# Performance work log

Measured on AMD Instinct MI355X. Metric: run time of the kernel, lower is better.

Reference implementation:

```python
import jax, jax.numpy as jnp
import numpy as np

WBITS = 4
ABITS = 8
OBITS = 8


def fwht(x):
    """Normalized fast Walsh-Hadamard transform along the last axis (n power of 2).
    Equivalent to matmul_hadU with had_K = I, K = 1 (n = 4096 = 2^12)."""
    shape = x.shape
    n = shape[-1]
    x = x.reshape(-1, n)
    h = 1
    while h < n:
        x = x.reshape(-1, n // (2 * h), 2, h)
        a, b = x[:, :, 0, :], x[:, :, 1, :]
        x = jnp.concatenate([a + b, a - b], axis=-1).reshape(-1, n)
        h *= 2
    inv_sqrt_n = jnp.asarray(1.0 / np.sqrt(n), x.dtype)
    return (x * inv_sqrt_n).reshape(shape)


def sym_fake_quant(t, bits, axis):
    """Symmetric min-max RTN fake quantization (per-channel for weights,
    per-token for activations)."""
    qmax = jnp.asarray(2.0 ** (bits - 1) - 1.0, t.dtype)
    scale = jnp.max(jnp.abs(t), axis=axis, keepdims=True) / qmax
    scale = jnp.maximum(scale, jnp.asarray(1e-8, t.dtype))
    q = jnp.clip(jnp.round(t / scale), -qmax, qmax)
    return q * scale


def setup_inputs() -> dict:
    key = jax.random.key(0)
    k1, k2, k3 = jax.random.split(key, 3)
    B, S, DIN, DOUT = 4, 2048, 4096, 4096
    return {
        "input": jax.random.normal(k1, (B, S, DIN), dtype=jnp.float32),
        "weight": jax.random.normal(k2, (DOUT, DIN), dtype=jnp.float32) * 0.02,
        "bias": jax.random.normal(k3, (DOUT,), dtype=jnp.float32) * 0.01,
    }


def reference(input, weight, bias):
    # online full Hadamard rotation of activations
    x = fwht(input)
    # activation quant (per-token, symmetric int8 fake-quant)
    x = sym_fake_quant(x, ABITS, axis=-1)
    # weight quant (per-output-channel, symmetric int4 fake-quant)
    w = sym_fake_quant(weight, WBITS, axis=-1)
    # F.linear: x @ w.T + b
    out = jnp.einsum("bsi,oi->bso", x, w) + bias
    # output quant (per-token, symmetric int8 fake-quant)
    out = sym_fake_quant(out, OBITS, axis=-1)
    return out
```

## Files before the change

kernel.cpp:

```cpp
#include <hip/hip_runtime.h>
#include <hip/hip_bf16.h>

#define DIN 4096
#define DOUT 4096
#define NROWS 8192

typedef int i32x4 __attribute__((ext_vector_type(4)));

__device__ __forceinline__ float block_absmax(float m, float* red) {
  #pragma unroll
  for (int off = 32; off > 0; off >>= 1)
    m = fmaxf(m, __shfl_down(m, off));
  const int tid = threadIdx.x;
  if ((tid & 63) == 0) red[tid >> 6] = m;
  __syncthreads();
  return fmaxf(fmaxf(red[0], red[1]), fmaxf(red[2], red[3]));
}

__global__ __launch_bounds__(256) void fwht_quant_kernel(
    const float* __restrict__ in, char* __restrict__ qx,
    float* __restrict__ sx) {
  __shared__ float buf[DIN];
  __shared__ float red[4];
  const int tid = threadIdx.x;
  const size_t row = blockIdx.x;
  const float4* src = (const float4*)(in + row * DIN);
  float4* b4 = (float4*)buf;
  for (int i = tid; i < DIN / 4; i += 256) b4[i] = src[i];
  __syncthreads();
  for (int h = 1; h < DIN; h <<= 1) {
    #pragma unroll
    for (int s = 0; s < 8; ++s) {
      int t = tid + s * 256;
      int i0 = ((t & ~(h - 1)) << 1) | (t & (h - 1));
      int i1 = i0 + h;
      float a = buf[i0], b = buf[i1];
      buf[i0] = a + b;
      buf[i1] = a - b;
    }
    __syncthreads();
  }
  const float inv = 0.015625f;
  float m = 0.0f;
  for (int i = tid; i < DIN / 4; i += 256) {
    float4 v = b4[i];
    m = fmaxf(m, fmaxf(fmaxf(fabsf(v.x), fabsf(v.y)),
                       fmaxf(fabsf(v.z), fabsf(v.w))));
  }
  float mx = block_absmax(m, red) * inv;
  float scale = fmaxf(mx / 127.0f, 1e-8f);
  if (tid == 0) sx[row] = scale;
  char* dst = qx + row * DIN;
  const float rs = 1.0f / scale;
  for (int i0 = tid * 4; i0 < DIN; i0 += 1024) {
    char4 pk;
    float q0 = fminf(fmaxf(rintf((buf[i0 + 0] * inv) * rs), -127.f), 127.f);
    float q1 = fminf(fmaxf(rintf((buf[i0 + 1] * inv) * rs), -127.f), 127.f);
    float q2 = fminf(fmaxf(rintf((buf[i0 + 2] * inv) * rs), -127.f), 127.f);
    float q3 = fminf(fmaxf(rintf((buf[i0 + 3] * inv) * rs), -127.f), 127.f);
    pk.x = (char)q0; pk.y = (char)q1; pk.z = (char)q2; pk.w = (char)q3;
    *(char4*)(dst + i0) = pk;
  }
}

__global__ __launch_bounds__(256) void wquant_kernel(
    const float* __restrict__ w, char* __restrict__ qw,
    float* __restrict__ sw) {
  __shared__ float buf[DIN];
  __shared__ float red[4];
  const int tid = threadIdx.x;
  const size_t row = blockIdx.x;
  const float4* src = (const float4*)(w + row * DIN);
  float4* b4 = (float4*)buf;
  float m = 0.0f;
  for (int i = tid; i < DIN / 4; i += 256) {
    float4 v = src[i];
    b4[i] = v;
    m = fmaxf(m, fmaxf(fmaxf(fabsf(v.x), fabsf(v.y)),
                       fmaxf(fabsf(v.z), fabsf(v.w))));
  }
  float mx = block_absmax(m, red);
  float scale = fmaxf(mx / 7.0f, 1e-8f);
  if (tid == 0) sw[row] = scale;
  char* dst = qw + row * DIN;
  const float rs = 1.0f / scale;
  for (int i0 = tid * 4; i0 < DIN; i0 += 1024) {
    char4 pk;
    float q0 = fminf(fmaxf(rintf(buf[i0 + 0] * rs), -7.f), 7.f);
    float q1 = fminf(fmaxf(rintf(buf[i0 + 1] * rs), -7.f), 7.f);
    float q2 = fminf(fmaxf(rintf(buf[i0 + 2] * rs), -7.f), 7.f);
    float q3 = fminf(fmaxf(rintf(buf[i0 + 3] * rs), -7.f), 7.f);
    pk.x = (char)q0; pk.y = (char)q1; pk.z = (char)q2; pk.w = (char)q3;
    *(char4*)(dst + i0) = pk;
  }
}

__global__ __launch_bounds__(512, 2) void gemm_kernel(
    const char* __restrict__ A,
    const char* __restrict__ Bt,
    const float* __restrict__ sx, const float* __restrict__ sw,
    const float* __restrict__ bias, float* __restrict__ out) {
  __shared__ char lds[131072];
  const int tid = threadIdx.x;
  const int lane = tid & 63;
  const int wid = tid >> 6;
  const int wr = wid >> 2;
  const int wc = wid & 3;
  int bid = blockIdx.x;
  int swz = (bid & 7) * 64 + (bid >> 3);
  const int tm = swz >> 4;
  const int tn = swz & 15;
  const size_t row0 = (size_t)tm * 256;
  const size_t col0 = (size_t)tn * 256;
  const int slot0 = (((lane >> 4) ^ (lane & 7)) << 4);

  i32x4 acc[4][2][4] = {};
  i32x4 fb[4][2];
  i32x4 fa[2][2];

#define STAGE(MAT, GROW0, KT, LBASE)                                          \
  {                                                                           \
    _Pragma("unroll")                                                         \
    for (int j = 0; j < 2; ++j) {                                             \
      int chunk = j * 8 + wid;                                                \
      int rr = chunk * 8 + (lane >> 3);                                       \
      int cc = (KT) * 128 + (((lane & 7) ^ (lane >> 3)) << 4);                \
      const char* src = (MAT) + ((GROW0) + rr) * (size_t)DIN + cc;            \
      __builtin_amdgcn_global_load_lds(                                       \
          (const __attribute__((address_space(1))) void*)src,                 \
          (__attribute__((address_space(3))) void*)(lds + (LBASE) +           \
                                                    chunk * 1024),            \
          16, 0, 0);                                                          \
    }                                                                         \
  }
#define STAGE_A(P, HALF, KT) \
  STAGE(A, row0 + (HALF) * 128, KT, (P) * 32768 + (HALF) * 16384)
#define STAGE_B(P, HALF, KT) \
  STAGE(Bt, col0 + (HALF) * 128, KT, 65536 + (P) * 32768 + (HALF) * 16384)

#define DS_A(Q, P)                                                            \
  {                                                                           \
    _Pragma("unroll")                                                         \
    for (int mm = 0; mm < 2; ++mm) {                                          \
      int ar = (Q) * 64 + wr * 32 + mm * 16 + (lane & 15);                    \
      _Pragma("unroll")                                                       \
      for (int kk = 0; kk < 2; ++kk)                                          \
        fa[mm][kk] =                                                          \
            *(const i32x4*)(lds + (P) * 32768 + ar * 128 + (slot0 ^ (kk * 64))); \
    }                                                                         \
  }
#define DS_B(P)                                                               \
  {                                                                           \
    _Pragma("unroll")                                                         \
    for (int nn = 0; nn < 4; ++nn) {                                          \
      int br = wc * 64 + nn * 16 + (lane & 15);                               \
      _Pragma("unroll")                                                       \
      for (int kk = 0; kk < 2; ++kk)                                          \
        fb[nn][kk] = *(const i32x4*)(lds + 65536 + (P) * 32768 + br * 128 +   \
                                     (slot0 ^ (kk * 64)));                    \
    }                                                                         \
  }
#define MFMA16(Q)                                                             \
  {                                                                           \
    __builtin_amdgcn_s_setprio(1);                                            \
    _Pragma("unroll")                                                         \
    for (int kk = 0; kk < 2; ++kk)                                            \
      _Pragma("unroll")                                                       \
      for (int mm = 0; mm < 2; ++mm)                                          \
        _Pragma("unroll")                                                     \
        for (int nn = 0; nn < 4; ++nn)                                        \
          acc[Q][mm][nn] = __builtin_amdgcn_mfma_i32_16x16x64_i8(             \
              fa[mm][kk], fb[nn][kk], acc[Q][mm][nn], 0, 0, 0);               \
    __builtin_amdgcn_s_setprio(0);                                            \
  }
#define BAR() __builtin_amdgcn_s_barrier()
#define WAIT_LGKM0() asm volatile("s_waitcnt lgkmcnt(0)" ::: "memory")

  STAGE_B(0, 0, 0); STAGE_B(0, 1, 0); STAGE_A(0, 0, 0); STAGE_A(0, 1, 0);
  STAGE_B(1, 0, 1); STAGE_B(1, 1, 1); STAGE_A(1, 0, 1);
  asm volatile("s_waitcnt vmcnt(6)" ::: "memory");
  BAR();

  #pragma unroll 1
  for (int i = 0; i < 16; ++i) {
    const int a = 2 * i, b = 2 * i + 1;
    const bool nl = (i < 15);
    DS_A(0, 0); DS_B(0);
    STAGE_A(1, 1, b);
    asm volatile("s_waitcnt lgkmcnt(8)" ::: "memory");
    BAR(); WAIT_LGKM0();
    MFMA16(0);
    BAR();
    DS_A(1, 0);
    if (nl) STAGE_B(0, 0, a + 2);
    BAR(); WAIT_LGKM0();
    MFMA16(1);
    BAR();
    DS_A(2, 0);
    if (nl) STAGE_B(0, 1, a + 2);
    BAR(); WAIT_LGKM0();
    MFMA16(2);
    BAR();
    DS_A(3, 0);
    if (nl) STAGE_A(0, 0, a + 2);
    BAR(); WAIT_LGKM0();
    MFMA16(3);
    if (nl) { asm volatile("s_waitcnt vmcnt(6)" ::: "memory"); }
    else    { asm volatile("s_waitcnt vmcnt(0)" ::: "memory"); }
    BAR();
    DS_A(0, 1); DS_B(1);
    if (nl) STAGE_A(0, 1, a + 2);
    asm volatile("s_waitcnt lgkmcnt(8)" ::: "memory");
    BAR(); WAIT_LGKM0();
    MFMA16(0);
    BAR();
    DS_A(1, 1);
    if (nl) STAGE_B(1, 0, b + 2);
    BAR(); WAIT_LGKM0();
    MFMA16(1);
    BAR();
    DS_A(2, 1);
    if (nl) STAGE_B(1, 1, b + 2);
    BAR(); WAIT_LGKM0();
    MFMA16(2);
    BAR();
    DS_A(3, 1);
    if (nl) STAGE_A(1, 0, b + 2);
    BAR(); WAIT_LGKM0();
    MFMA16(3);
    if (nl) { asm volatile("s_waitcnt vmcnt(6)" ::: "memory"); }
    BAR();
  }

  float swv[4], bv[4];
  #pragma unroll
  for (int nn = 0; nn < 4; ++nn) {
    size_t gc = col0 + wc * 64 + nn * 16 + (lane & 15);
    swv[nn] = sw[gc];
    bv[nn] = bias[gc];
  }
  #pragma unroll
  for (int q = 0; q < 4; ++q) {
    #pragma unroll
    for (int mm = 0; mm < 2; ++mm) {
      #pragma unroll
      for (int j = 0; j < 4; ++j) {
        size_t gr = row0 + q * 64 + wr * 32 + mm * 16 + ((lane >> 4) << 2) + j;
        float sxr = sx[gr];
        float* orow = out + gr * DOUT + col0 + wc * 64 + (lane & 15);
        #pragma unroll
        for (int nn = 0; nn < 4; ++nn)
          orow[nn * 16] = (float)acc[q][mm][nn][j] * (sxr * swv[nn]) + bv[nn];
      }
    }
  }
#undef STAGE
#undef STAGE_A
#undef STAGE_B
#undef DS_A
#undef DS_B
#undef MFMA16
#undef BAR
#undef WAIT_LGKM0
}

__global__ __launch_bounds__(256) void rowquant_kernel(float* __restrict__ out) {
  __shared__ float buf[DOUT];
  __shared__ float red[4];
  const int tid = threadIdx.x;
  const size_t row = blockIdx.x;
  float4* g4 = (float4*)(out + row * DOUT);
  float4* b4 = (float4*)buf;
  float m = 0.0f;
  for (int i = tid; i < DOUT / 4; i += 256) {
    float4 v = g4[i];
    b4[i] = v;
    m = fmaxf(m, fmaxf(fmaxf(fabsf(v.x), fabsf(v.y)),
                       fmaxf(fabsf(v.z), fabsf(v.w))));
  }
  float mx = block_absmax(m, red);
  float scale = fmaxf(mx / 127.0f, 1e-8f);
  for (int i = tid; i < DOUT / 4; i += 256) {
    float4 v = b4[i];
    v.x = fminf(fmaxf(rintf(v.x / scale), -127.0f), 127.0f) * scale;
    v.y = fminf(fmaxf(rintf(v.y / scale), -127.0f), 127.0f) * scale;
    v.z = fminf(fmaxf(rintf(v.z / scale), -127.0f), 127.0f) * scale;
    v.w = fminf(fmaxf(rintf(v.w / scale), -127.0f), 127.0f) * scale;
    g4[i] = v;
  }
}

extern "C" void kernel_launch(void* const* d_in, const int* in_sizes, int n_in,
                              void* d_out, int out_size, void* d_ws, size_t ws_size,
                              hipStream_t stream) {
  (void)in_sizes; (void)n_in; (void)out_size; (void)ws_size;
  const float* input = (const float*)d_in[0];
  const float* weight = (const float*)d_in[1];
  const float* bias = (const float*)d_in[2];
  float* out = (float*)d_out;
  char* ws = (char*)d_ws;
  char* qx = ws;
  char* qw = ws + ((size_t)32 << 20);
  float* sx = (float*)(ws + ((size_t)48 << 20));
  float* sw = (float*)(ws + ((size_t)48 << 20) + ((size_t)32 << 10));

  fwht_quant_kernel<<<NROWS, 256, 0, stream>>>(input, qx, sx);
  wquant_kernel<<<DOUT, 256, 0, stream>>>(weight, qw, sw);
  gemm_kernel<<<512, 512, 0, stream>>>(qx, qw, sx, sw, bias, out);
  rowquant_kernel<<<NROWS, 256, 0, stream>>>(out);
}
```

Before: 264.6 us.

## Register-resident radix-16 FWHT, coarser GEMM phases, register rowquant

```diff
diff --git a/kernel.cpp b/kernel.cpp
--- a/kernel.cpp
+++ b/kernel.cpp
@@ -20,47 +20,71 @@
 __global__ __launch_bounds__(256) void fwht_quant_kernel(
     const float* __restrict__ in, char* __restrict__ qx,
     float* __restrict__ sx) {
-  __shared__ float buf[DIN];
+  __shared__ float lds[4352];
   __shared__ float red[4];
   const int tid = threadIdx.x;
   const size_t row = blockIdx.x;
+  const int th = tid >> 4, tl = tid & 15;
+  float v[16];
+
   const float4* src = (const float4*)(in + row * DIN);
-  float4* b4 = (float4*)buf;
-  for (int i = tid; i < DIN / 4; i += 256) b4[i] = src[i];
+  #pragma unroll
+  for (int k = 0; k < 4; ++k) {
+    float4 f = src[tid * 4 + k];
+    v[4 * k + 0] = f.x; v[4 * k + 1] = f.y;
+    v[4 * k + 2] = f.z; v[4 * k + 3] = f.w;
+  }
+  #pragma unroll
+  for (int hb = 1; hb < 16; hb <<= 1)
+    #pragma unroll
+    for (int j = 0; j < 16; ++j)
+      if (!(j & hb)) {
+        float a0 = v[j], b0 = v[j | hb];
+        v[j] = a0 + b0; v[j | hb] = a0 - b0;
+      }
+  #pragma unroll
+  for (int j = 0; j < 16; ++j) lds[17 * tid + j] = v[j];
   __syncthreads();
-  for (int h = 1; h < DIN; h <<= 1) {
+  #pragma unroll
+  for (int j = 0; j < 16; ++j) v[j] = lds[272 * th + 17 * j + tl];
+  #pragma unroll
+  for (int hb = 1; hb < 16; hb <<= 1)
     #pragma unroll
-    for (int s = 0; s < 8; ++s) {
-      int t = tid + s * 256;
-      int i0 = ((t & ~(h - 1)) << 1) | (t & (h - 1));
-      int i1 = i0 + h;
-      float a = buf[i0], b = buf[i1];
-      buf[i0] = a + b;
-      buf[i1] = a - b;
-    }
-    __syncthreads();
-  }
-  const float inv = 0.015625f;
+    for (int j = 0; j < 16; ++j)
+      if (!(j & hb)) {
+        float a0 = v[j], b0 = v[j | hb];
+        v[j] = a0 + b0; v[j | hb] = a0 - b0;
+      }
+  #pragma unroll
+  for (int j = 0; j < 16; ++j) lds[272 * th + 17 * j + tl] = v[j];
+  __syncthreads();
+  #pragma unroll
+  for (int j = 0; j < 16; ++j) v[j] = lds[272 * j + 17 * th + tl];
+  #pragma unroll
+  for (int hb = 1; hb < 16; hb <<= 1)
+    #pragma unroll
+    for (int j = 0; j < 16; ++j)
+      if (!(j & hb)) {
+        float a0 = v[j], b0 = v[j | hb];
+        v[j] = a0 + b0; v[j | hb] = a0 - b0;
+      }
   float m = 0.0f;
-  for (int i = tid; i < DIN / 4; i += 256) {
-    float4 v = b4[i];
-    m = fmaxf(m, fmaxf(fmaxf(fabsf(v.x), fabsf(v.y)),
-                       fmaxf(fabsf(v.z), fabsf(v.w))));
-  }
-  float mx = block_absmax(m, red) * inv;
+  #pragma unroll
+  for (int j = 0; j < 16; ++j) m = fmaxf(m, fabsf(v[j]));
+  #pragma unroll
+  for (int j = 0; j < 16; ++j) lds[272 * j + 17 * th + tl] = v[j];
+  float mx = block_absmax(m, red) * 0.015625f;
   float scale = fmaxf(mx / 127.0f, 1e-8f);
   if (tid == 0) sx[row] = scale;
-  char* dst = qx + row * DIN;
   const float rs = 1.0f / scale;
-  for (int i0 = tid * 4; i0 < DIN; i0 += 1024) {
-    char4 pk;
-    float q0 = fminf(fmaxf(rintf((buf[i0 + 0] * inv) * rs), -127.f), 127.f);
-    float q1 = fminf(fmaxf(rintf((buf[i0 + 1] * inv) * rs), -127.f), 127.f);
-    float q2 = fminf(fmaxf(rintf((buf[i0 + 2] * inv) * rs), -127.f), 127.f);
-    float q3 = fminf(fmaxf(rintf((buf[i0 + 3] * inv) * rs), -127.f), 127.f);
-    pk.x = (char)q0; pk.y = (char)q1; pk.z = (char)q2; pk.w = (char)q3;
-    *(char4*)(dst + i0) = pk;
-  }
+  char pk[16];
+  #pragma unroll
+  for (int j = 0; j < 16; ++j) {
+    float q = fminf(fmaxf(rintf((lds[17 * tid + j] * 0.015625f) * rs), -127.f),
+                    127.f);
+    pk[j] = (char)q;
+  }
+  *(int4*)(qx + row * DIN + (size_t)tid * 16) = *(const int4*)pk;
 }
 
 __global__ __launch_bounds__(256) void wquant_kernel(
@@ -116,7 +140,7 @@
 
   i32x4 acc[4][2][4] = {};
   i32x4 fb[4][2];
-  i32x4 fa[2][2];
+  i32x4 fa[2][2][2];
 
 #define STAGE(MAT, GROW0, KT, LBASE)                                          \
   {                                                                           \
@@ -138,15 +162,18 @@
 #define STAGE_B(P, HALF, KT) \
   STAGE(Bt, col0 + (HALF) * 128, KT, 65536 + (P) * 32768 + (HALF) * 16384)
 
-#define DS_A(Q, P)                                                            \
+#define DS_A2(Q0, P)                                                          \
   {                                                                           \
     _Pragma("unroll")                                                         \
-    for (int mm = 0; mm < 2; ++mm) {                                          \
-      int ar = (Q) * 64 + wr * 32 + mm * 16 + (lane & 15);                    \
+    for (int s = 0; s < 2; ++s) {                                             \
       _Pragma("unroll")                                                       \
-      for (int kk = 0; kk < 2; ++kk)                                          \
-        fa[mm][kk] =                                                          \
-            *(const i32x4*)(lds + (P) * 32768 + ar * 128 + (slot0 ^ (kk * 64))); \
+      for (int mm = 0; mm < 2; ++mm) {                                        \
+        int ar = ((Q0) + s) * 64 + wr * 32 + mm * 16 + (lane & 15);           \
+        _Pragma("unroll")                                                     \
+        for (int kk = 0; kk < 2; ++kk)                                        \
+          fa[s][mm][kk] = *(const i32x4*)(lds + (P) * 32768 + ar * 128 +      \
+                                          (slot0 ^ (kk * 64)));               \
+      }                                                                       \
     }                                                                         \
   }
 #define DS_B(P)                                                               \
@@ -160,17 +187,19 @@
                                      (slot0 ^ (kk * 64)));                    \
     }                                                                         \
   }
-#define MFMA16(Q)                                                             \
+#define MFMA32(Q0)                                                            \
   {                                                                           \
     __builtin_amdgcn_s_setprio(1);                                            \
     _Pragma("unroll")                                                         \
     for (int kk = 0; kk < 2; ++kk)                                            \
       _Pragma("unroll")                                                       \
-      for (int mm = 0; mm < 2; ++mm)                                          \
+      for (int s = 0; s < 2; ++s)                                             \
         _Pragma("unroll")                                                     \
-        for (int nn = 0; nn < 4; ++nn)                                        \
-          acc[Q][mm][nn] = __builtin_amdgcn_mfma_i32_16x16x64_i8(             \
-              fa[mm][kk], fb[nn][kk], acc[Q][mm][nn], 0, 0, 0);               \
+        for (int mm = 0; mm < 2; ++mm)                                        \
+          _Pragma("unroll")                                                   \
+          for (int nn = 0; nn < 4; ++nn)                                      \
+            acc[(Q0) + s][mm][nn] = __builtin_amdgcn_mfma_i32_16x16x64_i8(    \
+                fa[s][mm][kk], fb[nn][kk], acc[(Q0) + s][mm][nn], 0, 0, 0);   \
     __builtin_amdgcn_s_setprio(0);                                            \
   }
 #define BAR() __builtin_amdgcn_s_barrier()
@@ -185,49 +214,29 @@
   for (int i = 0; i < 16; ++i) {
     const int a = 2 * i, b = 2 * i + 1;
     const bool nl = (i < 15);
-    DS_A(0, 0); DS_B(0);
+    DS_A2(0, 0); DS_B(0);
     STAGE_A(1, 1, b);
     asm volatile("s_waitcnt lgkmcnt(8)" ::: "memory");
     BAR(); WAIT_LGKM0();
-    MFMA16(0);
+    MFMA32(0);
     BAR();
-    DS_A(1, 0);
-    if (nl) STAGE_B(0, 0, a + 2);
+    DS_A2(2, 0);
+    if (nl) { STAGE_B(0, 0, a + 2); STAGE_B(0, 1, a + 2); STAGE_A(0, 0, a + 2); }
     BAR(); WAIT_LGKM0();
-    MFMA16(1);
-    BAR();
-    DS_A(2, 0);
-    if (nl) STAGE_B(0, 1, a + 2);
-    BAR(); WAIT_LGKM0();
-    MFMA16(2);
-    BAR();
-    DS_A(3, 0);
-    if (nl) STAGE_A(0, 0, a + 2);
-    BAR(); WAIT_LGKM0();
-    MFMA16(3);
+    MFMA32(2);
     if (nl) { asm volatile("s_waitcnt vmcnt(6)" ::: "memory"); }
     else    { asm volatile("s_waitcnt vmcnt(0)" ::: "memory"); }
     BAR();
-    DS_A(0, 1); DS_B(1);
+    DS_A2(0, 1); DS_B(1);
     if (nl) STAGE_A(0, 1, a + 2);
     asm volatile("s_waitcnt lgkmcnt(8)" ::: "memory");
     BAR(); WAIT_LGKM0();
-    MFMA16(0);
+    MFMA32(0);
     BAR();
-    DS_A(1, 1);
-    if (nl) STAGE_B(1, 0, b + 2);
+    DS_A2(2, 1);
+    if (nl) { STAGE_B(1, 0, b + 2); STAGE_B(1, 1, b + 2); STAGE_A(1, 0, b + 2); }
     BAR(); WAIT_LGKM0();
-    MFMA16(1);
-    BAR();
-    DS_A(2, 1);
-    if (nl) STAGE_B(1, 1, b + 2);
-    BAR(); WAIT_LGKM0();
-    MFMA16(2);
-    BAR();
-    DS_A(3, 1);
-    if (nl) STAGE_A(1, 0, b + 2);
-    BAR(); WAIT_LGKM0();
-    MFMA16(3);
+    MFMA32(2);
     if (nl) { asm volatile("s_waitcnt vmcnt(6)" ::: "memory"); }
     BAR();
   }
@@ -257,36 +266,36 @@
 #undef STAGE
 #undef STAGE_A
 #undef STAGE_B
-#undef DS_A
+#undef DS_A2
 #undef DS_B
-#undef MFMA16
+#undef MFMA32
 #undef BAR
 #undef WAIT_LGKM0
 }
 
 __global__ __launch_bounds__(256) void rowquant_kernel(float* __restrict__ out) {
-  __shared__ float buf[DOUT];
   __shared__ float red[4];
   const int tid = threadIdx.x;
   const size_t row = blockIdx.x;
   float4* g4 = (float4*)(out + row * DOUT);
-  float4* b4 = (float4*)buf;
+  float4 v[4];
   float m = 0.0f;
-  for (int i = tid; i < DOUT / 4; i += 256) {
-    float4 v = g4[i];
-    b4[i] = v;
-    m = fmaxf(m, fmaxf(fmaxf(fabsf(v.x), fabsf(v.y)),
-                       fmaxf(fabsf(v.z), fabsf(v.w))));
+  #pragma unroll
+  for (int k = 0; k < 4; ++k) {
+    v[k] = g4[tid + k * 256];
+    m = fmaxf(m, fmaxf(fmaxf(fabsf(v[k].x), fabsf(v[k].y)),
+                       fmaxf(fabsf(v[k].z), fabsf(v[k].w))));
   }
   float mx = block_absmax(m, red);
   float scale = fmaxf(mx / 127.0f, 1e-8f);
-  for (int i = tid; i < DOUT / 4; i += 256) {
-    float4 v = b4[i];
-    v.x = fminf(fmaxf(rintf(v.x / scale), -127.0f), 127.0f) * scale;
-    v.y = fminf(fmaxf(rintf(v.y / scale), -127.0f), 127.0f) * scale;
-    v.z = fminf(fmaxf(rintf(v.z / scale), -127.0f), 127.0f) * scale;
-    v.w = fminf(fmaxf(rintf(v.w / scale), -127.0f), 127.0f) * scale;
-    g4[i] = v;
+  #pragma unroll
+  for (int k = 0; k < 4; ++k) {
+    float4 w = v[k];
+    w.x = fminf(fmaxf(rintf(w.x / scale), -127.0f), 127.0f) * scale;
+    w.y = fminf(fmaxf(rintf(w.y / scale), -127.0f), 127.0f) * scale;
+    w.z = fminf(fmaxf(rintf(w.z / scale), -127.0f), 127.0f) * scale;
+    w.w = fminf(fmaxf(rintf(w.w / scale), -127.0f), 127.0f) * scale;
+    g4[tid + k * 256] = w;
   }
 }
 
```

After: 225.1 us. 1.18x faster.
